# Kernel optimization log

Measured on AMD Instinct MI355X. Metric: run time of the kernel, lower is better.

The kernel has to match this reference:

```python
import jax, jax.numpy as jnp
import numpy as np

B, S, D = 64, 512, 512  # bias broadcast and final bmm force S == input_dim == dim_v
DK, DV = 512, 512


def setup_inputs() -> dict:
    key = jax.random.key(0)
    ks = jax.random.split(key, 16)
    sc = 0.02
    inp = {
        "sent_emb": jax.random.normal(ks[0], (B, S, D), jnp.float32),
        "pos_emb": jax.random.normal(ks[1], (B, S, D), jnp.float32),
        "branch_emb": jax.random.normal(ks[2], (B, S, D), jnp.float32),
        # Linear weights stored torch-style: [out, in]
        "Wq": jax.random.normal(ks[3], (DK, D), jnp.float32) * sc,
        "bq": jnp.zeros((DK,), jnp.float32),
        "Wk": jax.random.normal(ks[4], (DK, D), jnp.float32) * sc,
        "bk": jnp.zeros((DK,), jnp.float32),
        "Wv": jax.random.normal(ks[5], (DV, D), jnp.float32) * sc,
        "bv": jnp.zeros((DV,), jnp.float32),
        "Wpq": jax.random.normal(ks[6], (D, D), jnp.float32) * sc,
        "bpq": jnp.zeros((D,), jnp.float32),
        "Wpk": jax.random.normal(ks[7], (D, D), jnp.float32) * sc,
        "bpk": jnp.zeros((D,), jnp.float32),
        "bias": jax.random.normal(ks[8], (D,), jnp.float32) * sc,
    }
    return inp


def reference(sent_emb, pos_emb, branch_emb, Wq, bq, Wk, bk, Wv, bv, Wpq, bpq, Wpk, bpk, bias):
    d = sent_emb.shape[-1]
    norm = 1.0 / jnp.sqrt(jnp.asarray(2.0 * d, sent_emb.dtype))
    # projections (torch Linear: x @ W.T + b)
    Q = sent_emb @ Wq.T + bq          # [B,S,DK]
    K = sent_emb @ Wk.T + bk          # [B,S,DK]
    V = sent_emb @ Wv.T + bv          # [B,S,DV]
    Uq = pos_emb @ Wpq.T + bpq        # [B,S,D]
    Uk = pos_emb @ Wpk.T + bpk        # [B,S,D]
    text_score = jnp.einsum('bsd,btd->bst', Q, K) * norm   # [B,S,S]
    pos_score = jnp.einsum('bsd,btd->bst', Uq, Uk) * norm  # [B,S,S]
    att = text_score + pos_score + bias                    # bias [D] broadcasts over last axis (S==D)
    att_softmax = jax.nn.softmax(att, axis=2)
    # torch.bmm(att, V.permute(0,2,1)): out[b,i,j] = sum_t att[b,i,t] * V[b,j,t]
    output = jnp.einsum('bit,bjt->bij', att_softmax, V)    # [B,S,S] (DV==S)
    return (att_softmax, output)
```

## Files before the change

kernel.cpp:

```cpp
#include <hip/hip_runtime.h>

typedef unsigned short u16;
typedef unsigned int   u32;
typedef __bf16 bf16x8 __attribute__((ext_vector_type(8)));
typedef float  f32x4  __attribute__((ext_vector_type(4)));

#define BATCH 64
#define SEQ   512
#define BSS   (64 * 512 * 512)
#define MTOT  (64 * 512)

__device__ __forceinline__ u16 f2bf(float f) {
  u32 u = __builtin_bit_cast(u32, f);
  u += 0x7FFFu + ((u >> 16) & 1u);
  return (u16)(u >> 16);
}

__device__ __forceinline__ void gl16(const void* g, void* l) {
  __builtin_amdgcn_global_load_lds(
      (__attribute__((address_space(1))) void*)g,
      (__attribute__((address_space(3))) void*)l,
      16, 0, 0);
}

__global__ __launch_bounds__(256) void cvt2_bf16_kernel(
    const float* __restrict__ in0, u16* __restrict__ out0,
    const float* __restrict__ in1, u16* __restrict__ out1, int n8) {
  int i = blockIdx.x * 256 + threadIdx.x;
  const float* in = in0;
  u16* out = out0;
  if (i >= n8) { i -= n8; in = in1; out = out1; }
  const float4* p = reinterpret_cast<const float4*>(in) + (size_t)i * 2;
  float4 x = p[0], y = p[1];
  uint4 r;
  r.x = (u32)f2bf(x.x) | ((u32)f2bf(x.y) << 16);
  r.y = (u32)f2bf(x.z) | ((u32)f2bf(x.w) << 16);
  r.z = (u32)f2bf(y.x) | ((u32)f2bf(y.y) << 16);
  r.w = (u32)f2bf(y.z) | ((u32)f2bf(y.w) << 16);
  reinterpret_cast<uint4*>(out)[i] = r;
}

__global__ __launch_bounds__(256) void pack_w_kernel(
    const float* __restrict__ wq, const float* __restrict__ wk,
    const float* __restrict__ wv, const float* __restrict__ wpq,
    const float* __restrict__ wpk, u16* __restrict__ wc1, u16* __restrict__ wc2) {
  int i = blockIdx.x * 256 + threadIdx.x;
  int which = i >> 18;
  int off = i & 262143;
  const float* src = which == 0 ? wq : which == 1 ? wk : which == 2 ? wv
                   : which == 3 ? wpq : wpk;
  u16 h = f2bf(src[off]);
  if (which < 3) wc1[(size_t)which * 262144 + off] = h;
  else           wc2[(size_t)(which - 3) * 262144 + off] = h;
}

__global__ __launch_bounds__(256) void pack_bias_kernel(
    const float* __restrict__ bq, const float* __restrict__ bk,
    const float* __restrict__ bv, const float* __restrict__ bpq,
    const float* __restrict__ bpk, float* __restrict__ b1, float* __restrict__ b2) {
  int i = blockIdx.x * 256 + threadIdx.x;
  if (i < 1536) {
    b1[i] = i < 512 ? bq[i] : i < 1024 ? bk[i - 512] : bv[i - 1024];
  } else {
    int j = i - 1536;
    b2[j] = j < 512 ? bpq[j] : bpk[j - 512];
  }
}

template <int MODE>
__global__ __launch_bounds__(512, 4) void gemm_db(
    const u16* __restrict__ A, const u16* __restrict__ Bm,
    u16* __restrict__ U0, u16* __restrict__ U1, u16* __restrict__ U2,
    const float* __restrict__ bias, float* __restrict__ F) {
  __shared__ u16 ls[2 * 12288];

  const int t = threadIdx.x;

  const int gx = gridDim.x, gy = gridDim.y;
  int id = (blockIdx.z * gy + blockIdx.y) * gx + blockIdx.x;
  const int q = (gx * gy * gridDim.z) >> 3;
  id = (id & 7) * q + (id >> 3);
  const int bx = id % gx;
  const int rem = id / gx;
  const int by = rem % gy;
  const int z = rem / gy;

  const int m0 = by * 256;
  const int n0 = bx * 128;
  const int K = 512;

  const u16* Ab = A + (MODE == 2 ? (size_t)z * 262144 : 0);
  const u16* Bb = Bm + (MODE == 2 ? (size_t)z * 262144 : 0);
  float* Fb = (MODE == 2) ? (F + (size_t)z * 262144) : F;

  const int u = (t & 7) ^ ((t >> 3) & 7);
  const int srow = 2 * (t >> 3) + (u & 1);
  const int scol = (u >> 1) * 8;
  const u16* gA = Ab + (size_t)(m0 + srow) * K + scol;
  const u16* gB = Bb + (size_t)(n0 + srow) * K + scol;

  const int l = t & 63;
  const int w = t >> 6;
  const int wm = (w & 3) * 64;
  const int wn = (w >> 2) * 64;
  const int fr = l & 15;

  const int sOff = ((2 * (l >> 4) + (fr & 1)) ^ (fr >> 1)) << 4;
  const int aoffB = (((wm + fr) & ~1) << 6) + sOff;
  const int boffB = 16384 + (((wn + fr) & ~1) << 6) + sOff;

  f32x4 acc[4][4];
#pragma unroll
  for (int i = 0; i < 4; ++i)
#pragma unroll
    for (int j = 0; j < 4; ++j) acc[i][j] = (f32x4){0.f, 0.f, 0.f, 0.f};

  {
    char* Ld = (char*)ls + t * 16;
    gl16(gA, Ld);
    gl16(gA + (size_t)128 * K, Ld + 8192);
    gl16(gB, Ld + 16384);
  }
  __syncthreads();

  int cur = 0;
  for (int it = 0; it < 16; ++it) {
    if (it < 15) {
      const int k0 = (it + 1) * 32;
      char* Ld = (char*)ls + (cur ^ 1) * 24576 + t * 16;
      gl16(gA + k0, Ld);
      gl16(gA + (size_t)128 * K + k0, Ld + 8192);
      gl16(gB + k0, Ld + 16384);
    }
    const char* Lc = (const char*)ls + cur * 24576;
    bf16x8 af[4], bfv[4];
#pragma unroll
    for (int mt = 0; mt < 4; ++mt)
      af[mt] = *reinterpret_cast<const bf16x8*>(Lc + aoffB + mt * 1024);
#pragma unroll
    for (int nt = 0; nt < 4; ++nt)
      bfv[nt] = *reinterpret_cast<const bf16x8*>(Lc + boffB + nt * 1024);
#pragma unroll
    for (int mt = 0; mt < 4; ++mt)
#pragma unroll
      for (int nt = 0; nt < 4; ++nt)
        acc[mt][nt] = __builtin_amdgcn_mfma_f32_16x16x32_bf16(
            af[mt], bfv[nt], acc[mt][nt], 0, 0, 0);
    __syncthreads();
    cur ^= 1;
  }

  const int cr = (l >> 4) * 4;
  const int cc = l & 15;
#pragma unroll
  for (int mt = 0; mt < 4; ++mt) {
#pragma unroll
    for (int nt = 0; nt < 4; ++nt) {
      const int col = n0 + wn + nt * 16 + cc;
#pragma unroll
      for (int r = 0; r < 4; ++r) {
        const int row = m0 + wm + mt * 16 + cr + r;
        float v = acc[mt][nt][r];
        if (MODE == 2) {
          Fb[(size_t)row * 512 + col] = v;
        } else {
          v += bias[col];
          u16 h = f2bf(v);
          const int which = col >> 9, c = col & 511;
          if (MODE == 0) {
            if (which == 0)      U0[(size_t)row * 1024 + c] = h;
            else if (which == 1) U1[(size_t)row * 1024 + c] = h;
            else                 U2[(size_t)row * 512 + c] = h;
          } else {
            if (which == 0) U0[(size_t)row * 1024 + 512 + c] = h;
            else            U1[(size_t)row * 1024 + 512 + c] = h;
          }
        }
      }
    }
  }
}

__global__ __launch_bounds__(512, 4) void score_softmax(
    const u16* __restrict__ QU, const u16* __restrict__ KU,
    const float* __restrict__ bias, float* __restrict__ attF,
    u16* __restrict__ attB) {
  __shared__ u16 lsA[64 * 256];
  __shared__ float sred[64 * 8];

  const int t = threadIdx.x;
  const int b = blockIdx.x;
  const int rg = blockIdx.y;
  const int l = t & 63;
  const int w = t >> 6;
  const int wn = w * 64;
  const int fr = l & 15;
  const int fkb = (l >> 4) * 16;
  const int cc = l & 15;
  const int cr = (l >> 4) * 4;
  const int sw = (l & 7) << 4;

  const int browA = b * 512 + rg * 64;

  const int stg_colb = ((t & 31) << 4) ^ (((t >> 5) & 7) << 4);
  const char* gAc = (const char*)QU + (size_t)(browA + (t >> 5)) * 2048 + stg_colb;

  const u16* gK = KU + (size_t)(b * 512 + wn + fr) * 1024 + (l >> 4) * 8;

  float bc[4];
#pragma unroll
  for (int nt = 0; nt < 4; ++nt) bc[nt] = bias[wn + nt * 16 + cc];

  f32x4 acc[4][4];
#pragma unroll
  for (int i = 0; i < 4; ++i)
#pragma unroll
    for (int j = 0; j < 4; ++j) acc[i][j] = (f32x4){0.f, 0.f, 0.f, 0.f};

#pragma unroll
  for (int c = 0; c < 4; ++c) {
    __syncthreads();
#pragma unroll
    for (int i = 0; i < 4; ++i)
      gl16(gAc + c * 512 + (size_t)i * 16 * 2048,
           (char*)lsA + t * 16 + (size_t)i * 8192);
    __syncthreads();

#pragma unroll 2
    for (int kk = 0; kk < 8; ++kk) {
      bf16x8 af[4], bfg[4];
#pragma unroll
      for (int nt = 0; nt < 4; ++nt)
        bfg[nt] = *reinterpret_cast<const bf16x8*>(
            gK + (size_t)nt * 16 * 1024 + c * 256 + kk * 32);
#pragma unroll
      for (int mt = 0; mt < 4; ++mt)
        af[mt] = *reinterpret_cast<const bf16x8*>(
            (const char*)lsA + (mt * 16 + fr) * 512 + ((kk * 64 + fkb) ^ sw));
#pragma unroll
      for (int mt = 0; mt < 4; ++mt)
#pragma unroll
        for (int nt = 0; nt < 4; ++nt)
          acc[mt][nt] = __builtin_amdgcn_mfma_f32_16x16x32_bf16(
              af[mt], bfg[nt], acc[mt][nt], 0, 0, 0);
    }
  }

#pragma unroll
  for (int mt = 0; mt < 4; ++mt)
#pragma unroll
    for (int nt = 0; nt < 4; ++nt)
#pragma unroll
      for (int r = 0; r < 4; ++r)
        acc[mt][nt][r] = acc[mt][nt][r] * 0.03125f + bc[nt];

  float rm[4][4];
#pragma unroll
  for (int mt = 0; mt < 4; ++mt)
#pragma unroll
    for (int r = 0; r < 4; ++r) {
      float m = fmaxf(fmaxf(acc[mt][0][r], acc[mt][1][r]),
                      fmaxf(acc[mt][2][r], acc[mt][3][r]));
#pragma unroll
      for (int s = 1; s < 16; s <<= 1) m = fmaxf(m, __shfl_xor(m, s, 64));
      rm[mt][r] = m;
    }
  if (cc == 0) {
#pragma unroll
    for (int mt = 0; mt < 4; ++mt)
#pragma unroll
      for (int r = 0; r < 4; ++r)
        sred[(mt * 16 + cr + r) * 8 + w] = rm[mt][r];
  }
  __syncthreads();
#pragma unroll
  for (int mt = 0; mt < 4; ++mt)
#pragma unroll
    for (int r = 0; r < 4; ++r) {
      const float* p = &sred[(mt * 16 + cr + r) * 8];
      f32x4 a = *reinterpret_cast<const f32x4*>(p);
      f32x4 c = *reinterpret_cast<const f32x4*>(p + 4);
      rm[mt][r] = fmaxf(fmaxf(fmaxf(a[0], a[1]), fmaxf(a[2], a[3])),
                        fmaxf(fmaxf(c[0], c[1]), fmaxf(c[2], c[3])));
    }
  __syncthreads();

  float rs[4][4];
#pragma unroll
  for (int mt = 0; mt < 4; ++mt)
#pragma unroll
    for (int r = 0; r < 4; ++r) {
      float s = 0.f;
#pragma unroll
      for (int nt = 0; nt < 4; ++nt) {
        float e = __expf(acc[mt][nt][r] - rm[mt][r]);
        acc[mt][nt][r] = e;
        s += e;
      }
#pragma unroll
      for (int sh = 1; sh < 16; sh <<= 1) s += __shfl_xor(s, sh, 64);
      rs[mt][r] = s;
    }
  if (cc == 0) {
#pragma unroll
    for (int mt = 0; mt < 4; ++mt)
#pragma unroll
      for (int r = 0; r < 4; ++r)
        sred[(mt * 16 + cr + r) * 8 + w] = rs[mt][r];
  }
  __syncthreads();
#pragma unroll
  for (int mt = 0; mt < 4; ++mt)
#pragma unroll
    for (int r = 0; r < 4; ++r) {
      const float* p = &sred[(mt * 16 + cr + r) * 8];
      f32x4 a = *reinterpret_cast<const f32x4*>(p);
      f32x4 c = *reinterpret_cast<const f32x4*>(p + 4);
      rs[mt][r] = 1.0f / ((a[0] + a[1]) + (a[2] + a[3]) +
                          (c[0] + c[1]) + (c[2] + c[3]));
    }

  float* aF = attF + (size_t)b * 262144 + (size_t)rg * 64 * 512;
  u16* aB = attB + (size_t)b * 262144 + (size_t)rg * 64 * 512;
#pragma unroll
  for (int mt = 0; mt < 4; ++mt)
#pragma unroll
    for (int nt = 0; nt < 4; ++nt)
#pragma unroll
      for (int r = 0; r < 4; ++r) {
        const size_t idx = (size_t)(mt * 16 + cr + r) * 512 + wn + nt * 16 + cc;
        float a = acc[mt][nt][r] * rs[mt][r];
        aF[idx] = a;
        aB[idx] = f2bf(a);
      }
}

extern "C" void kernel_launch(void* const* d_in, const int* in_sizes, int n_in,
                              void* d_out, int out_size, void* d_ws,
                              size_t ws_size, hipStream_t stream) {
  const float* sent = (const float*)d_in[0];
  const float* pos  = (const float*)d_in[1];
  const float* Wq  = (const float*)d_in[3];
  const float* bq  = (const float*)d_in[4];
  const float* Wk  = (const float*)d_in[5];
  const float* bk  = (const float*)d_in[6];
  const float* Wv  = (const float*)d_in[7];
  const float* bv  = (const float*)d_in[8];
  const float* Wpq = (const float*)d_in[9];
  const float* bpq = (const float*)d_in[10];
  const float* Wpk = (const float*)d_in[11];
  const float* bpk = (const float*)d_in[12];
  const float* abias = (const float*)d_in[13];
  float* out = (float*)d_out;

  char* ws = (char*)d_ws;
  u16* Xs   = (u16*)(ws);
  u16* Xp   = (u16*)(ws + 33554432ul);
  u16* QU   = (u16*)(ws + 67108864ul);
  u16* KU   = (u16*)(ws + 134217728ul);
  u16* Vb   = (u16*)(ws + 201326592ul);
  u16* attB = (u16*)(ws + 234881024ul);
  u16* Wc1  = (u16*)(ws + 268435456ul);
  u16* Wc2  = (u16*)(ws + 270008320ul);
  float* b1 = (float*)(ws + 271056896ul);
  float* b2 = (float*)(ws + 271063040ul);

  float* attF = out;
  float* out2 = out + BSS;

  cvt2_bf16_kernel<<<16384, 256, 0, stream>>>(sent, Xs, pos, Xp, MTOT * 512 / 8);
  pack_w_kernel<<<5120, 256, 0, stream>>>(Wq, Wk, Wv, Wpq, Wpk, Wc1, Wc2);
  pack_bias_kernel<<<10, 256, 0, stream>>>(bq, bk, bv, bpq, bpk, b1, b2);

  gemm_db<0><<<dim3(12, 128, 1), 512, 0, stream>>>(Xs, Wc1, QU, KU, Vb, b1, nullptr);
  gemm_db<1><<<dim3(8, 128, 1), 512, 0, stream>>>(Xp, Wc2, QU, KU, nullptr, b2, nullptr);

  score_softmax<<<dim3(BATCH, 8, 1), 512, 0, stream>>>(QU, KU, abias, attF, attB);

  gemm_db<2><<<dim3(4, 2, BATCH), 512, 0, stream>>>(attB, Vb, nullptr, nullptr,
                                                    nullptr, nullptr, out2);

  (void)in_sizes; (void)n_in; (void)out_size; (void)ws_size;
}
```

Measured before the change: 504.0 us.

## Fuse attention-times-V GEMM into score softmax kernel via LDS-resident probabilities

The separate attention@V GEMM launch is folded into the score/softmax kernel. Each block keeps its 64x512 bf16 probability tile in a swizzled 64 KB LDS buffer and multiplies it directly against V read from global memory, so the bf16 attention matrix is no longer written to and re-read from HBM. The K-operand loads in the score loop also become register double-buffered (prefetch next slice). The cost is larger LDS per block, which lowers occupancy, plus a longer per-block tail, while the second GEMM loses its own tuned LDS tiling.

```diff
diff --git a/kernel.cpp b/kernel.cpp
--- a/kernel.cpp
+++ b/kernel.cpp
@@ -181,12 +181,14 @@
   }
 }
 
-__global__ __launch_bounds__(512, 4) void score_softmax(
+__global__ __launch_bounds__(512, 4) void score_softmax_pv(
     const u16* __restrict__ QU, const u16* __restrict__ KU,
-    const float* __restrict__ bias, float* __restrict__ attF,
-    u16* __restrict__ attB) {
-  __shared__ u16 lsA[64 * 256];
+    const u16* __restrict__ Vb, const float* __restrict__ bias,
+    float* __restrict__ attF, float* __restrict__ out2) {
+  __shared__ u16 attS[64 * 512];
   __shared__ float sred[64 * 8];
+
+  u16* lsA = attS;
 
   const int t = threadIdx.x;
   const int b = blockIdx.x;
@@ -217,6 +219,11 @@
 #pragma unroll
     for (int j = 0; j < 4; ++j) acc[i][j] = (f32x4){0.f, 0.f, 0.f, 0.f};
 
+  bf16x8 bnow[4], bnxt[4];
+#pragma unroll
+  for (int nt = 0; nt < 4; ++nt)
+    bnow[nt] = *reinterpret_cast<const bf16x8*>(gK + (size_t)nt * 16384);
+
 #pragma unroll
   for (int c = 0; c < 4; ++c) {
     __syncthreads();
@@ -226,13 +233,16 @@
            (char*)lsA + t * 16 + (size_t)i * 8192);
     __syncthreads();
 
-#pragma unroll 2
+#pragma unroll
     for (int kk = 0; kk < 8; ++kk) {
-      bf16x8 af[4], bfg[4];
-#pragma unroll
-      for (int nt = 0; nt < 4; ++nt)
-        bfg[nt] = *reinterpret_cast<const bf16x8*>(
-            gK + (size_t)nt * 16 * 1024 + c * 256 + kk * 32);
+      const int ki = c * 8 + kk;
+      if (ki < 31) {
+#pragma unroll
+        for (int nt = 0; nt < 4; ++nt)
+          bnxt[nt] = *reinterpret_cast<const bf16x8*>(
+              gK + (size_t)nt * 16384 + (ki + 1) * 32);
+      }
+      bf16x8 af[4];
 #pragma unroll
       for (int mt = 0; mt < 4; ++mt)
         af[mt] = *reinterpret_cast<const bf16x8*>(
@@ -242,7 +252,9 @@
 #pragma unroll
         for (int nt = 0; nt < 4; ++nt)
           acc[mt][nt] = __builtin_amdgcn_mfma_f32_16x16x32_bf16(
-              af[mt], bfg[nt], acc[mt][nt], 0, 0, 0);
+              af[mt], bnow[nt], acc[mt][nt], 0, 0, 0);
+#pragma unroll
+      for (int nt = 0; nt < 4; ++nt) bnow[nt] = bnxt[nt];
     }
   }
 
@@ -321,18 +333,68 @@
     }
 
   float* aF = attF + (size_t)b * 262144 + (size_t)rg * 64 * 512;
-  u16* aB = attB + (size_t)b * 262144 + (size_t)rg * 64 * 512;
 #pragma unroll
   for (int mt = 0; mt < 4; ++mt)
 #pragma unroll
     for (int nt = 0; nt < 4; ++nt)
 #pragma unroll
       for (int r = 0; r < 4; ++r) {
-        const size_t idx = (size_t)(mt * 16 + cr + r) * 512 + wn + nt * 16 + cc;
+        const int row = mt * 16 + cr + r;
+        const int col = wn + nt * 16 + cc;
         float a = acc[mt][nt][r] * rs[mt][r];
-        aF[idx] = a;
-        aB[idx] = f2bf(a);
+        aF[(size_t)row * 512 + col] = a;
+        const int tg = (col >> 3) ^ (row & 7);
+        attS[row * 512 + tg * 8 + (col & 7)] = f2bf(a);
       }
+  __syncthreads();
+
+  const u16* gV = Vb + (size_t)(b * 512 + wn + fr) * 512 + (l >> 4) * 8;
+  f32x4 acc2[4][4];
+#pragma unroll
+  for (int i = 0; i < 4; ++i)
+#pragma unroll
+    for (int j = 0; j < 4; ++j) acc2[i][j] = (f32x4){0.f, 0.f, 0.f, 0.f};
+
+  bf16x8 vnow[4], vnxt[4];
+#pragma unroll
+  for (int nt = 0; nt < 4; ++nt)
+    vnow[nt] = *reinterpret_cast<const bf16x8*>(gV + (size_t)nt * 8192);
+
+#pragma unroll 2
+  for (int kk = 0; kk < 16; ++kk) {
+    if (kk < 15) {
+#pragma unroll
+      for (int nt = 0; nt < 4; ++nt)
+        vnxt[nt] = *reinterpret_cast<const bf16x8*>(
+            gV + (size_t)nt * 8192 + (kk + 1) * 32);
+    }
+    const int tg0 = kk * 4 + (l >> 4);
+    bf16x8 af2[4];
+#pragma unroll
+    for (int mt = 0; mt < 4; ++mt) {
+      const int row = mt * 16 + fr;
+      af2[mt] = *reinterpret_cast<const bf16x8*>(
+          attS + row * 512 + ((tg0 ^ (row & 7)) * 8));
+    }
+#pragma unroll
+    for (int mt = 0; mt < 4; ++mt)
+#pragma unroll
+      for (int nt = 0; nt < 4; ++nt)
+        acc2[mt][nt] = __builtin_amdgcn_mfma_f32_16x16x32_bf16(
+            af2[mt], vnow[nt], acc2[mt][nt], 0, 0, 0);
+#pragma unroll
+    for (int nt = 0; nt < 4; ++nt) vnow[nt] = vnxt[nt];
+  }
+
+  float* oF = out2 + (size_t)b * 262144 + (size_t)rg * 64 * 512;
+#pragma unroll
+  for (int mt = 0; mt < 4; ++mt)
+#pragma unroll
+    for (int nt = 0; nt < 4; ++nt)
+#pragma unroll
+      for (int r = 0; r < 4; ++r)
+        oF[(size_t)(mt * 16 + cr + r) * 512 + wn + nt * 16 + cc] =
+            acc2[mt][nt][r];
 }
 
 extern "C" void kernel_launch(void* const* d_in, const int* in_sizes, int n_in,
@@ -359,7 +421,6 @@
   u16* QU   = (u16*)(ws + 67108864ul);
   u16* KU   = (u16*)(ws + 134217728ul);
   u16* Vb   = (u16*)(ws + 201326592ul);
-  u16* attB = (u16*)(ws + 234881024ul);
   u16* Wc1  = (u16*)(ws + 268435456ul);
   u16* Wc2  = (u16*)(ws + 270008320ul);
   float* b1 = (float*)(ws + 271056896ul);
@@ -375,10 +436,8 @@
   gemm_db<0><<<dim3(12, 128, 1), 512, 0, stream>>>(Xs, Wc1, QU, KU, Vb, b1, nullptr);
   gemm_db<1><<<dim3(8, 128, 1), 512, 0, stream>>>(Xp, Wc2, QU, KU, nullptr, b2, nullptr);
 
-  score_softmax<<<dim3(BATCH, 8, 1), 512, 0, stream>>>(QU, KU, abias, attF, attB);
-
-  gemm_db<2><<<dim3(4, 2, BATCH), 512, 0, stream>>>(attB, Vb, nullptr, nullptr,
-                                                    nullptr, nullptr, out2);
+  score_softmax_pv<<<dim3(BATCH, 8, 1), 512, 0, stream>>>(QU, KU, Vb, abias,
+                                                          attF, out2);
 
   (void)in_sizes; (void)n_in; (void)out_size; (void)ws_size;
 }
```

After: 553.2 us. +9.8%, slower.
